# Kernel tuning notes

Measured on AMD Instinct MI355X. Metric: run time of the kernel, lower is better.

The kernel has to match this reference:

```python
import jax, jax.numpy as jnp
import numpy as np

N_NODES = 50000
N_EDGES = 800000
C = 64          # node channels (in_dim == out_dim)
CE = 32         # edge channels
NEG_SLOPE = 0.2


def setup_inputs() -> dict:
    key = jax.random.key(0)
    k1, k2, k3, k4, k5 = jax.random.split(key, 5)
    x = jax.random.normal(k1, (N_NODES, C), dtype=jnp.float32)
    edge_index = jax.random.randint(k2, (2, N_EDGES), 0, N_NODES, dtype=jnp.int64)
    edge_attr = jax.random.normal(k3, (N_EDGES, CE), dtype=jnp.float32)
    # parameters (kaiming-uniform-ish scale)
    wn_bound = float(np.sqrt(6.0 / C))
    weight_node = jax.random.uniform(k4, (C, C), minval=-wn_bound, maxval=wn_bound, dtype=jnp.float32)
    wa_bound = float(np.sqrt(6.0 / (2 * C + CE)))
    weight_triplet_att = jax.random.uniform(k5, (1, 2 * C + CE), minval=-wa_bound, maxval=wa_bound, dtype=jnp.float32)
    bias = jnp.zeros((C,), dtype=jnp.float32)
    return {"x": x, "edge_index": edge_index, "edge_attr": edge_attr,
            "weight_node": weight_node, "weight_triplet_att": weight_triplet_att, "bias": bias}


def reference(x, edge_index, edge_attr, weight_node, weight_triplet_att, bias):
    # x: [N, C], edge_index: [2, E] (row 0 = source j, row 1 = target i), edge_attr: [E, Ce]
    n_nodes = x.shape[0]
    xw = x @ weight_node                      # [N, C]
    src, dst = edge_index[0], edge_index[1]
    x_j = xw[src]                             # [E, C] messages from source
    x_i = xw[dst]                             # [E, C] target features
    triplet = jnp.concatenate([x_i, edge_attr, x_j], axis=-1)   # [E, 2C+Ce]
    alpha = (triplet * weight_triplet_att).sum(axis=-1)          # [E]
    alpha = jax.nn.leaky_relu(alpha, NEG_SLOPE)
    # segment softmax over edges grouped by destination node (PyG softmax)
    seg_max = jax.ops.segment_max(alpha, dst, num_segments=n_nodes)  # [N]
    alpha = jnp.exp(alpha - seg_max[dst])
    seg_sum = jax.ops.segment_sum(alpha, dst, num_segments=n_nodes)  # [N]
    alpha = alpha / (seg_sum[dst] + 1e-16)
    msg = alpha[:, None] * x_j                                      # [E, C]
    out = jax.ops.segment_sum(msg, dst, num_segments=n_nodes)       # [N, C]
    return out + bias
```

## Files before the change

kernel.cpp:

```cpp
#include <hip/hip_runtime.h>
#include <math.h>

#define N_NODES 50000
#define N_EDGES 800000
#define C 64
#define CE 32
#define NEG_SLOPE 0.2f

#define SCAN_BLOCK 256
#define SCAN_ELEMS 4
#define SCAN_TILE (SCAN_BLOCK * SCAN_ELEMS)
#define SCAN_SHIFT 10
#define SCAN_NBLOCKS ((N_NODES + SCAN_TILE - 1) / SCAN_TILE)

__device__ __forceinline__ unsigned bf16_rne(float f) {
    unsigned u = __float_as_uint(f);
    return (u + 0x7FFFu + ((u >> 16) & 1u)) >> 16;
}

__global__ __launch_bounds__(256) void k1_xw(
    const float* __restrict__ x, const float* __restrict__ W,
    const float* __restrict__ watt,
    unsigned short* __restrict__ xwb, float* __restrict__ a_i, float* __restrict__ a_j)
{
    __shared__ float Wl[64 * 64];
    __shared__ float xs[4][64];
    int tid = threadIdx.x;
    for (int i = tid; i < 64 * 64 / 4; i += 256)
        ((float4*)Wl)[i] = ((const float4*)W)[i];
    int warp = tid >> 6, lane = tid & 63;
    int row = blockIdx.x * 4 + warp;
    if (row < N_NODES) xs[warp][lane] = x[(size_t)row * C + lane];
    __syncthreads();
    if (row >= N_NODES) return;
    float acc = 0.f;
#pragma unroll
    for (int k = 0; k < 64; k++) acc += xs[warp][k] * Wl[k * 64 + lane];
    xwb[(size_t)row * C + lane] = (unsigned short)bf16_rne(acc);
    float vi = acc * watt[lane];
    float vj = acc * watt[96 + lane];
#pragma unroll
    for (int off = 32; off; off >>= 1) {
        vi += __shfl_down(vi, off, 64);
        vj += __shfl_down(vj, off, 64);
    }
    if (lane == 0) { a_i[row] = vi; a_j[row] = vj; }
}

__global__ __launch_bounds__(256) void k2_edge(
    const int* __restrict__ eidx, const float* __restrict__ edge_attr,
    const float* __restrict__ watt,
    const float* __restrict__ a_i, const float* __restrict__ a_j,
    float* __restrict__ wexp, unsigned* __restrict__ count,
    unsigned* __restrict__ erank)
{
    int e = blockIdx.x * 256 + threadIdx.x;
    if (e >= N_EDGES) return;
    int src = eidx[e];
    int dst = eidx[N_EDGES + e];
    const float4* ea = (const float4*)(edge_attr + (size_t)e * CE);
    float ec = 0.f;
#pragma unroll
    for (int k = 0; k < CE / 4; k++) {
        float4 v = ea[k];
        ec += v.x * watt[64 + 4 * k + 0] + v.y * watt[64 + 4 * k + 1] +
              v.z * watt[64 + 4 * k + 2] + v.w * watt[64 + 4 * k + 3];
    }
    float al = a_i[dst] + ec + a_j[src];
    al = al > 0.f ? al : NEG_SLOPE * al;
    wexp[e] = __expf(al);
    erank[e] = atomicAdd(&count[dst], 1u);
}

__global__ __launch_bounds__(SCAN_BLOCK) void k3a_blockscan(
    const unsigned* __restrict__ count, unsigned* __restrict__ base,
    unsigned* __restrict__ blocksum)
{
    __shared__ unsigned wsum[4];
    int tid = threadIdx.x, lane = tid & 63, warp = tid >> 6;
    int gbase = blockIdx.x * SCAN_TILE + tid * SCAN_ELEMS;
    unsigned v[SCAN_ELEMS];
    unsigned s = 0;
#pragma unroll
    for (int k = 0; k < SCAN_ELEMS; k++) {
        int i = gbase + k;
        v[k] = (i < N_NODES) ? count[i] : 0u;
        s += v[k];
    }
    unsigned inc = s;
#pragma unroll
    for (int off = 1; off < 64; off <<= 1) {
        unsigned t = __shfl_up(inc, off, 64);
        if (lane >= off) inc += t;
    }
    if (lane == 63) wsum[warp] = inc;
    __syncthreads();
    unsigned wpre = 0;
#pragma unroll
    for (int w = 0; w < 4; w++) if (w < warp) wpre += wsum[w];
    unsigned run = wpre + inc - s;
#pragma unroll
    for (int k = 0; k < SCAN_ELEMS; k++) {
        int i = gbase + k;
        if (i < N_NODES) base[i] = run;
        run += v[k];
    }
    if (tid == 255) blocksum[blockIdx.x] = wpre + inc;
}

__global__ __launch_bounds__(64) void k3b_scansums(unsigned* __restrict__ blocksum)
{
    int lane = threadIdx.x;
    unsigned v = (lane < SCAN_NBLOCKS) ? blocksum[lane] : 0u;
    unsigned inc = v;
#pragma unroll
    for (int off = 1; off < 64; off <<= 1) {
        unsigned t = __shfl_up(inc, off, 64);
        if (lane >= off) inc += t;
    }
    if (lane < SCAN_NBLOCKS) blocksum[lane] = inc - v;
}

__global__ __launch_bounds__(256) void k4_scatter(
    const int* __restrict__ eidx, const float* __restrict__ wexp,
    const unsigned* __restrict__ base, const unsigned* __restrict__ blocksum,
    const unsigned* __restrict__ erank, unsigned* __restrict__ sorted)
{
    int e = blockIdx.x * 256 + threadIdx.x;
    if (e >= N_EDGES) return;
    int src = eidx[e];
    int dst = eidx[N_EDGES + e];
    unsigned pk = ((unsigned)src << 16) | bf16_rne(wexp[e]);
    unsigned pos = base[dst] + blocksum[(unsigned)dst >> SCAN_SHIFT] + erank[e];
    sorted[pos] = pk;
}

__global__ __launch_bounds__(256) void k5_gather(
    const unsigned* __restrict__ base, const unsigned* __restrict__ blocksum,
    const unsigned* __restrict__ count, const unsigned* __restrict__ sorted,
    const unsigned short* __restrict__ xwb, const float* __restrict__ bias,
    float* __restrict__ out)
{
    int warp = threadIdx.x >> 6, lane = threadIdx.x & 63;
    int node = blockIdx.x * 4 + warp;
    if (node >= N_NODES) return;
    int group = lane >> 3, sub = lane & 7;
    unsigned b = base[node] + blocksum[(unsigned)node >> SCAN_SHIFT];
    unsigned c = count[node];
    float acc[8];
#pragma unroll
    for (int i = 0; i < 8; i++) acc[i] = 0.f;
    float wpart = 0.f;
    for (unsigned chunk = 0; chunk < c; chunk += 64) {
        unsigned m = min(64u, c - chunk);
        unsigned pk = 0u;
        if (lane < m) pk = sorted[b + chunk + lane];
        wpart += __uint_as_float(pk << 16);
        unsigned iters = (m + 7) >> 3;
        for (unsigned it = 0; it < iters; it++) {
            int t = (int)(it * 8) + group;
            unsigned p = (unsigned)__shfl((int)pk, t, 64);
            float w = __uint_as_float(p << 16);
            unsigned s = p >> 16;
            uint4 v = ((const uint4*)(xwb + (size_t)s * C))[sub];
            acc[0] += w * __uint_as_float(v.x << 16);
            acc[1] += w * __uint_as_float(v.x & 0xFFFF0000u);
            acc[2] += w * __uint_as_float(v.y << 16);
            acc[3] += w * __uint_as_float(v.y & 0xFFFF0000u);
            acc[4] += w * __uint_as_float(v.z << 16);
            acc[5] += w * __uint_as_float(v.z & 0xFFFF0000u);
            acc[6] += w * __uint_as_float(v.w << 16);
            acc[7] += w * __uint_as_float(v.w & 0xFFFF0000u);
        }
    }
#pragma unroll
    for (int off = 8; off < 64; off <<= 1) {
#pragma unroll
        for (int i = 0; i < 8; i++) acc[i] += __shfl_xor(acc[i], off, 64);
    }
#pragma unroll
    for (int off = 1; off < 64; off <<= 1)
        wpart += __shfl_xor(wpart, off, 64);
    float rden = 1.0f / (wpart + 1e-16f);
    if (group == 0) {
        float4 b4a = ((const float4*)bias)[sub * 2];
        float4 b4b = ((const float4*)bias)[sub * 2 + 1];
        float4 o1, o2;
        o1.x = acc[0] * rden + b4a.x; o1.y = acc[1] * rden + b4a.y;
        o1.z = acc[2] * rden + b4a.z; o1.w = acc[3] * rden + b4a.w;
        o2.x = acc[4] * rden + b4b.x; o2.y = acc[5] * rden + b4b.y;
        o2.z = acc[6] * rden + b4b.z; o2.w = acc[7] * rden + b4b.w;
        ((float4*)(out + (size_t)node * C))[sub * 2] = o1;
        ((float4*)(out + (size_t)node * C))[sub * 2 + 1] = o2;
    }
}

extern "C" void kernel_launch(void* const* d_in, const int* in_sizes, int n_in,
                              void* d_out, int out_size, void* d_ws, size_t ws_size,
                              hipStream_t stream) {
    const float* x         = (const float*)d_in[0];
    const int*   eidx      = (const int*)d_in[1];
    const float* edge_attr = (const float*)d_in[2];
    const float* W         = (const float*)d_in[3];
    const float* watt      = (const float*)d_in[4];
    const float* bias      = (const float*)d_in[5];
    float* out = (float*)d_out;

    char* ws = (char*)d_ws;
    size_t off = 0;
    auto alloc = [&](size_t bytes) -> void* {
        void* p = ws + off;
        off += (bytes + 255) & ~(size_t)255;
        return p;
    };
    unsigned short* xwb = (unsigned short*)alloc((size_t)N_NODES * C * 2);
    float*    a_i      = (float*)alloc(N_NODES * 4);
    float*    a_j      = (float*)alloc(N_NODES * 4);
    float*    wexp     = (float*)alloc(N_EDGES * 4);
    unsigned* erank    = (unsigned*)alloc(N_EDGES * 4);
    unsigned* sorted   = (unsigned*)alloc((size_t)N_EDGES * 4);
    unsigned* basep    = (unsigned*)alloc(N_NODES * 4);
    unsigned* blocksum = (unsigned*)alloc(SCAN_NBLOCKS * 4);
    unsigned* count    = (unsigned*)alloc(N_NODES * 4);

    hipMemsetAsync(count, 0, (size_t)N_NODES * 4, stream);

    k1_xw<<<(N_NODES + 3) / 4, 256, 0, stream>>>(x, W, watt, xwb, a_i, a_j);
    k2_edge<<<(N_EDGES + 255) / 256, 256, 0, stream>>>(eidx, edge_attr, watt, a_i, a_j,
                                                       wexp, count, erank);
    k3a_blockscan<<<SCAN_NBLOCKS, SCAN_BLOCK, 0, stream>>>(count, basep, blocksum);
    k3b_scansums<<<1, 64, 0, stream>>>(blocksum);
    k4_scatter<<<(N_EDGES + 255) / 256, 256, 0, stream>>>(eidx, wexp, basep, blocksum,
                                                          erank, sorted);
    k5_gather<<<(N_NODES + 3) / 4, 256, 0, stream>>>(basep, blocksum, count, sorted,
                                                     xwb, bias, out);
}
```

Baseline: 257.1 us.

## Coalesce edge-attr reads in edge kernel and pack scatter inputs

The edge kernel now assigns 8 threads per edge, so each thread loads one float4 of edge_attr and the partial dot products are reduced with shuffles. This makes the large edge_attr stream fully coalesced. One lane per edge then computes the attention weight and writes two packed words: src with the bf16 exp weight, and dst with the atomic rank. The scatter kernel reads only these two words instead of re-reading edge_index, wexp and erank, which cuts its traffic. In exchange the edge kernel launches 8x more threads, only 1/8 of them do the tail work, and dst and rank must each fit in 16 bits.

```diff
diff --git a/kernel.cpp b/kernel.cpp
--- a/kernel.cpp
+++ b/kernel.cpp
@@ -51,25 +51,33 @@
     const int* __restrict__ eidx, const float* __restrict__ edge_attr,
     const float* __restrict__ watt,
     const float* __restrict__ a_i, const float* __restrict__ a_j,
-    float* __restrict__ wexp, unsigned* __restrict__ count,
-    unsigned* __restrict__ erank)
-{
-    int e = blockIdx.x * 256 + threadIdx.x;
+    unsigned* __restrict__ packA, unsigned* __restrict__ packB,
+    unsigned* __restrict__ count)
+{
+    int tid = threadIdx.x;
+    int lane = tid & 63;
+    int sub = tid & 7;
+    int e = (blockIdx.x * 256 + tid) >> 3;
     if (e >= N_EDGES) return;
-    int src = eidx[e];
-    int dst = eidx[N_EDGES + e];
-    const float4* ea = (const float4*)(edge_attr + (size_t)e * CE);
-    float ec = 0.f;
-#pragma unroll
-    for (int k = 0; k < CE / 4; k++) {
-        float4 v = ea[k];
-        ec += v.x * watt[64 + 4 * k + 0] + v.y * watt[64 + 4 * k + 1] +
-              v.z * watt[64 + 4 * k + 2] + v.w * watt[64 + 4 * k + 3];
-    }
-    float al = a_i[dst] + ec + a_j[src];
-    al = al > 0.f ? al : NEG_SLOPE * al;
-    wexp[e] = __expf(al);
-    erank[e] = atomicAdd(&count[dst], 1u);
+    float4 v = ((const float4*)edge_attr)[(size_t)e * (CE / 4) + sub];
+    float4 wv = ((const float4*)(watt + 64))[sub];
+    float p = v.x * wv.x + v.y * wv.y + v.z * wv.z + v.w * wv.w;
+    p += __shfl_xor(p, 1, 64);
+    p += __shfl_xor(p, 2, 64);
+    p += __shfl_xor(p, 4, 64);
+    float myec = __shfl(p, (lane & 7) * 8, 64);
+    if (lane < 8) {
+        int eg = ((blockIdx.x * 256 + (tid & ~63)) >> 3) + lane;
+        if (eg < N_EDGES) {
+            int src = eidx[eg];
+            int dst = eidx[N_EDGES + eg];
+            float al = a_i[dst] + myec + a_j[src];
+            al = al > 0.f ? al : NEG_SLOPE * al;
+            packA[eg] = ((unsigned)src << 16) | bf16_rne(__expf(al));
+            unsigned r = atomicAdd(&count[dst], 1u);
+            packB[eg] = ((unsigned)dst << 16) | r;
+        }
+    }
 }
 
 __global__ __launch_bounds__(SCAN_BLOCK) void k3a_blockscan(
@@ -122,17 +130,16 @@
 }
 
 __global__ __launch_bounds__(256) void k4_scatter(
-    const int* __restrict__ eidx, const float* __restrict__ wexp,
+    const unsigned* __restrict__ packA, const unsigned* __restrict__ packB,
     const unsigned* __restrict__ base, const unsigned* __restrict__ blocksum,
-    const unsigned* __restrict__ erank, unsigned* __restrict__ sorted)
+    unsigned* __restrict__ sorted)
 {
     int e = blockIdx.x * 256 + threadIdx.x;
     if (e >= N_EDGES) return;
-    int src = eidx[e];
-    int dst = eidx[N_EDGES + e];
-    unsigned pk = ((unsigned)src << 16) | bf16_rne(wexp[e]);
-    unsigned pos = base[dst] + blocksum[(unsigned)dst >> SCAN_SHIFT] + erank[e];
-    sorted[pos] = pk;
+    unsigned pa = packA[e];
+    unsigned pb = packB[e];
+    unsigned d = pb >> 16;
+    sorted[base[d] + blocksum[d >> SCAN_SHIFT] + (pb & 0xFFFFu)] = pa;
 }
 
 __global__ __launch_bounds__(256) void k5_gather(
@@ -216,8 +223,8 @@
     unsigned short* xwb = (unsigned short*)alloc((size_t)N_NODES * C * 2);
     float*    a_i      = (float*)alloc(N_NODES * 4);
     float*    a_j      = (float*)alloc(N_NODES * 4);
-    float*    wexp     = (float*)alloc(N_EDGES * 4);
-    unsigned* erank    = (unsigned*)alloc(N_EDGES * 4);
+    unsigned* packA    = (unsigned*)alloc(N_EDGES * 4);
+    unsigned* packB    = (unsigned*)alloc(N_EDGES * 4);
     unsigned* sorted   = (unsigned*)alloc((size_t)N_EDGES * 4);
     unsigned* basep    = (unsigned*)alloc(N_NODES * 4);
     unsigned* blocksum = (unsigned*)alloc(SCAN_NBLOCKS * 4);
@@ -226,12 +233,12 @@
     hipMemsetAsync(count, 0, (size_t)N_NODES * 4, stream);
 
     k1_xw<<<(N_NODES + 3) / 4, 256, 0, stream>>>(x, W, watt, xwb, a_i, a_j);
-    k2_edge<<<(N_EDGES + 255) / 256, 256, 0, stream>>>(eidx, edge_attr, watt, a_i, a_j,
-                                                       wexp, count, erank);
+    k2_edge<<<(N_EDGES * 8) / 256, 256, 0, stream>>>(eidx, edge_attr, watt, a_i, a_j,
+                                                     packA, packB, count);
     k3a_blockscan<<<SCAN_NBLOCKS, SCAN_BLOCK, 0, stream>>>(count, basep, blocksum);
     k3b_scansums<<<1, 64, 0, stream>>>(blocksum);
-    k4_scatter<<<(N_EDGES + 255) / 256, 256, 0, stream>>>(eidx, wexp, basep, blocksum,
-                                                          erank, sorted);
+    k4_scatter<<<(N_EDGES + 255) / 256, 256, 0, stream>>>(packA, packB, basep,
+                                                          blocksum, sorted);
     k5_gather<<<(N_NODES + 3) / 4, 256, 0, stream>>>(basep, blocksum, count, sorted,
                                                      xwb, bias, out);
 }
```

Result: no change. 260.3 us (+1.2%).
